# Performance work log

Hardware: AMD Instinct MI355X
Metric: run time of the kernel (lower is better)

Reference implementation:

```python
import jax, jax.numpy as jnp
import numpy as np

B, C, H, W = 4, 64, 64, 64

def setup_inputs() -> dict:
    key = jax.random.key(0)
    ks = jax.random.split(key, 9)
    return {
        "x": jax.random.normal(ks[0], (B, C, H, W), dtype=jnp.float32),
        "Wq": jax.random.normal(ks[1], (C, C), dtype=jnp.float32) * (1.0 / np.sqrt(C)),
        "bq": jax.random.normal(ks[2], (C,), dtype=jnp.float32) * 0.02,
        "Wk": jax.random.normal(ks[3], (C, C), dtype=jnp.float32) * (1.0 / np.sqrt(C)),
        "bk": jax.random.normal(ks[4], (C,), dtype=jnp.float32) * 0.02,
        "Wv": jax.random.normal(ks[5], (C, C), dtype=jnp.float32) * (1.0 / np.sqrt(C)),
        "bv": jax.random.normal(ks[6], (C,), dtype=jnp.float32) * 0.02,
        "rel_h": jax.random.normal(ks[7], (1, C, H, 1), dtype=jnp.float32),
        "rel_w": jax.random.normal(ks[8], (1, C, 1, W), dtype=jnp.float32),
    }

def reference(x, Wq, bq, Wk, bk, Wv, bv, rel_h, rel_w):
    b, c, h, w = x.shape
    n = h * w
    xf = x.reshape(b, c, n)                                  # [B,C,N]
    # 1x1 convs == channel-wise linear maps (weight [out,in])
    q = jnp.einsum('oc,bcn->bno', Wq, xf) + bq               # [B,N,C]
    k = jnp.einsum('oc,bcn->bon', Wk, xf) + bk[:, None]      # [B,C,N]
    v = jnp.einsum('oc,bcn->bon', Wv, xf) + bv[:, None]      # [B,C,N]
    energy = jnp.einsum('bnc,bcm->bnm', q, k)                # content term [B,N,N]
    pos = (rel_h + rel_w).reshape(c, n)                      # [C,N]
    energy = energy + jnp.einsum('bnc,cm->bnm', q, pos)      # add positional bias
    attn = jax.nn.softmax(energy, axis=-1)                   # [B,N,N]
    # out[b,c,n] = sum_m v[b,c,m] * attn[b,n,m]  (bmm with attention^T)
    out = jnp.einsum('bcm,bnm->bcn', v, attn)
    return out.reshape(b, c, h, w)
```

## Files before the change

### kernel.cpp

```cpp
#include <hip/hip_runtime.h>
#include <math.h>

#define NPOS 4096
#define NB   4
#define NROW (NB * NPOS)
#define LOG2E 1.44269504088896f

typedef _Float16 f16;
typedef f16 f16x4 __attribute__((ext_vector_type(4)));
typedef f16 f16x8 __attribute__((ext_vector_type(8)));
typedef float f32x4 __attribute__((ext_vector_type(4)));

#define LDW 72

__global__ __launch_bounds__(256) void qkv_proj(
    const float* __restrict__ x,
    const float* __restrict__ Wq, const float* __restrict__ bq,
    const float* __restrict__ Wk, const float* __restrict__ bk,
    const float* __restrict__ Wv, const float* __restrict__ bv,
    const float* __restrict__ rel_h, const float* __restrict__ rel_w,
    f16* __restrict__ qh, f16* __restrict__ kh, f16* __restrict__ vh)
{
    __shared__ __align__(16) f16 Ws[192 * LDW];
    __shared__ __align__(16) f16 Xs[32 * LDW];
    __shared__ __align__(16) f16 Vs[64 * 36];

    const int tid = threadIdx.x;
    const int b   = blockIdx.x >> 7;
    const int n0  = (blockIdx.x & 127) << 5;

    #pragma unroll
    for (int k = 0; k < 12; ++k) {
        int idx  = tid + k * 256;
        int orow = idx >> 4;
        int cseg = (idx & 15) << 2;
        int mat  = orow >> 6;
        int o    = orow & 63;
        const float* wsrc = (mat == 0) ? Wq : ((mat == 1) ? Wk : Wv);
        float4 v = *(const float4*)(wsrc + o * 64 + cseg);
        f16x4 h; h[0] = (f16)v.x; h[1] = (f16)v.y; h[2] = (f16)v.z; h[3] = (f16)v.w;
        *(f16x4*)(&Ws[orow * LDW + cseg]) = h;
    }
    {
        int c  = tid >> 2;
        int ns = (tid & 3) << 3;
        const float* xp = x + ((size_t)(b * 64 + c)) * NPOS + n0 + ns;
        float4 v0 = *(const float4*)(xp);
        float4 v1 = *(const float4*)(xp + 4);
        Xs[(ns + 0) * LDW + c] = (f16)v0.x;
        Xs[(ns + 1) * LDW + c] = (f16)v0.y;
        Xs[(ns + 2) * LDW + c] = (f16)v0.z;
        Xs[(ns + 3) * LDW + c] = (f16)v0.w;
        Xs[(ns + 4) * LDW + c] = (f16)v1.x;
        Xs[(ns + 5) * LDW + c] = (f16)v1.y;
        Xs[(ns + 6) * LDW + c] = (f16)v1.z;
        Xs[(ns + 7) * LDW + c] = (f16)v1.w;
    }
    __syncthreads();

    const int wave = tid >> 6;
    const int lane = tid & 63;
    const int quad = lane >> 4;
    const int l16  = lane & 15;
    const int rg   = wave >> 1;
    const int tb   = (wave & 1) * 6;

    const f16x8 a0 = *(const f16x8*)(&Xs[(rg * 16 + l16) * LDW + quad * 8]);
    const f16x8 a1 = *(const f16x8*)(&Xs[(rg * 16 + l16) * LDW + 32 + quad * 8]);

    f32x4 acc[6];
    #pragma unroll
    for (int i = 0; i < 6; ++i) {
        int t = tb + i;
        f32x4 c0 = {0, 0, 0, 0};
        f16x8 b0 = *(const f16x8*)(&Ws[(t * 16 + l16) * LDW + quad * 8]);
        f16x8 b1 = *(const f16x8*)(&Ws[(t * 16 + l16) * LDW + 32 + quad * 8]);
        c0 = __builtin_amdgcn_mfma_f32_16x16x32_f16(a0, b0, c0, 0, 0, 0);
        c0 = __builtin_amdgcn_mfma_f32_16x16x32_f16(a1, b1, c0, 0, 0, 0);
        acc[i] = c0;
    }

    #pragma unroll
    for (int i = 0; i < 6; ++i) {
        int t = tb + i;
        if (t < 4) {
            int o = t * 16 + l16;
            float bb = bq[o];
            #pragma unroll
            for (int r = 0; r < 4; ++r) {
                size_t n = (size_t)b * NPOS + n0 + rg * 16 + quad * 4 + r;
                qh[n * 64 + o] = (f16)((acc[i][r] + bb) * LOG2E);
            }
        } else if (t < 8) {
            int o = (t - 4) * 16 + l16;
            int h = n0 >> 6;
            int wbase = (n0 & 63) + rg * 16;
            float bb = bk[o] + rel_h[o * 64 + h];
            #pragma unroll
            for (int r = 0; r < 4; ++r) {
                size_t n = (size_t)b * NPOS + n0 + rg * 16 + quad * 4 + r;
                kh[n * 64 + o] = (f16)(acc[i][r] + bb + rel_w[o * 64 + wbase + quad * 4 + r]);
            }
        } else {
            int o = (t - 8) * 16 + l16;
            float bb = bv[o];
            #pragma unroll
            for (int r = 0; r < 4; ++r)
                Vs[o * 36 + rg * 16 + quad * 4 + r] = (f16)(acc[i][r] + bb);
        }
    }
    __syncthreads();
    {
        int c  = tid >> 2;
        int ns = (tid & 3) << 3;
        f16x8 vv = *(const f16x8*)(&Vs[c * 36 + ns]);
        *(f16x8*)(vh + ((size_t)(b * 64 + c)) * NPOS + n0 + ns) = vv;
    }
}

#define LDP 72

__global__ __launch_bounds__(256, 4) void attn(
    const f16* __restrict__ qh, const f16* __restrict__ kh,
    const f16* __restrict__ vh,
    f16* __restrict__ Op, float* __restrict__ Mp, float* __restrict__ Lp,
    int split, int mchunk)
{
    __shared__ __align__(16) f16 Ks[2][64 * LDP];
    __shared__ __align__(16) f16 Vt[2][64 * LDP];

    const int tid  = threadIdx.x;
    const int wave = tid >> 6;
    const int lane = tid & 63;
    const int quad = lane >> 4;
    const int l16  = lane & 15;
    const int s    = blockIdx.x % split;
    const int tile = blockIdx.x / split;
    const int b    = tile >> 5;
    const int n0   = (tile & 31) << 7;

    f16x8 bq0[2], bq1[2];
    #pragma unroll
    for (int g = 0; g < 2; ++g) {
        const f16* qbase = qh + ((size_t)b * NPOS + n0 + wave * 32 + g * 16 + l16) * 64;
        bq0[g] = *(const f16x8*)(qbase + quad * 8);
        bq1[g] = *(const f16x8*)(qbase + 32 + quad * 8);
    }

    f32x4 O[2][4] = {{{0,0,0,0},{0,0,0,0},{0,0,0,0},{0,0,0,0}},
                     {{0,0,0,0},{0,0,0,0},{0,0,0,0},{0,0,0,0}}};
    float m_i[2] = {-1e30f, -1e30f}, l_i[2] = {0.f, 0.f};

    const int srow = tid >> 2;
    const int sseg = (tid & 3) * 16;
    const f16* kb = kh + (size_t)b * NPOS * 64;
    const f16* vb = vh + (size_t)b * 64 * NPOS;

    const int m_begin = s * mchunk;
    for (int m0 = m_begin; m0 < m_begin + mchunk; m0 += 128) {
        #pragma unroll
        for (int h = 0; h < 2; ++h) {
            const f16* ksrc = kb + (size_t)(m0 + h * 64 + srow) * 64 + sseg;
            *(f16x8*)(&Ks[h][srow * LDP + sseg])     = *(const f16x8*)(ksrc);
            *(f16x8*)(&Ks[h][srow * LDP + sseg + 8]) = *(const f16x8*)(ksrc + 8);
            const f16* vsrc = vb + (size_t)srow * NPOS + m0 + h * 64 + sseg;
            *(f16x8*)(&Vt[h][srow * LDP + sseg])     = *(const f16x8*)(vsrc);
            *(f16x8*)(&Vt[h][srow * LDP + sseg + 8]) = *(const f16x8*)(vsrc + 8);
        }
        __syncthreads();

        #pragma unroll
        for (int h = 0; h < 2; ++h) {
            f32x4 S[2][4];
            #pragma unroll
            for (int t = 0; t < 4; ++t) {
                f16x8 ak0 = *(const f16x8*)(&Ks[h][(t * 16 + l16) * LDP + quad * 8]);
                f16x8 ak1 = *(const f16x8*)(&Ks[h][(t * 16 + l16) * LDP + 32 + quad * 8]);
                #pragma unroll
                for (int g = 0; g < 2; ++g) {
                    f32x4 acc = {0, 0, 0, 0};
                    acc = __builtin_amdgcn_mfma_f32_16x16x32_f16(ak0, bq0[g], acc, 0, 0, 0);
                    acc = __builtin_amdgcn_mfma_f32_16x16x32_f16(ak1, bq1[g], acc, 0, 0, 0);
                    S[g][t] = acc;
                }
            }

            f16x4 pa[2][4];
            #pragma unroll
            for (int g = 0; g < 2; ++g) {
                float mx = S[g][0][0];
                #pragma unroll
                for (int t = 0; t < 4; ++t)
                    #pragma unroll
                    for (int r = 0; r < 4; ++r) mx = fmaxf(mx, S[g][t][r]);
                mx = fmaxf(mx, __shfl_xor(mx, 16));
                mx = fmaxf(mx, __shfl_xor(mx, 32));

                if (__any(mx > m_i[g])) {
                    float mnew  = fmaxf(m_i[g], mx);
                    float alpha = __builtin_amdgcn_exp2f(m_i[g] - mnew);
                    m_i[g] = mnew;
                    l_i[g] *= alpha;
                    #pragma unroll
                    for (int r = 0; r < 4; ++r) {
                        float av = __shfl(alpha, quad * 20 + r);
                        O[g][0][r] *= av; O[g][1][r] *= av;
                        O[g][2][r] *= av; O[g][3][r] *= av;
                    }
                }

                float rs = 0.f;
                #pragma unroll
                for (int t = 0; t < 4; ++t) {
                    f16x4 a;
                    #pragma unroll
                    for (int r = 0; r < 4; ++r) {
                        float e = __builtin_amdgcn_exp2f(S[g][t][r] - m_i[g]);
                        rs += e;
                        a[r] = (f16)e;
                    }
                    pa[g][t] = a;
                }
                rs += __shfl_xor(rs, 16);
                rs += __shfl_xor(rs, 32);
                l_i[g] += rs;
            }

            #pragma unroll
            for (int u = 0; u < 4; ++u) {
                #pragma unroll
                for (int t = 0; t < 4; ++t) {
                    f16x4 bf = *(const f16x4*)(&Vt[h][(u * 16 + l16) * LDP + t * 16 + quad * 4]);
                    O[0][u] = __builtin_amdgcn_mfma_f32_16x16x16f16(pa[0][t], bf, O[0][u], 0, 0, 0);
                    O[1][u] = __builtin_amdgcn_mfma_f32_16x16x16f16(pa[1][t], bf, O[1][u], 0, 0, 0);
                }
            }
        }
        __syncthreads();
    }

    #pragma unroll
    for (int g = 0; g < 2; ++g) {
        #pragma unroll
        for (int r = 0; r < 4; ++r) {
            float lr  = __shfl(l_i[g], quad * 20 + r);
            float inv = 1.f / lr;
            size_t row = (size_t)b * NPOS + n0 + wave * 32 + g * 16 + quad * 4 + r;
            #pragma unroll
            for (int u = 0; u < 4; ++u)
                Op[((size_t)s * NROW + row) * 64 + u * 16 + l16] = (f16)(O[g][u][r] * inv);
        }
        if (lane < 16) {
            size_t row = (size_t)b * NPOS + n0 + wave * 32 + g * 16 + l16;
            Mp[(size_t)s * NROW + row] = m_i[g];
            Lp[(size_t)s * NROW + row] = l_i[g];
        }
    }
}

__global__ __launch_bounds__(256) void combine(
    const f16* __restrict__ Op, const float* __restrict__ Mp,
    const float* __restrict__ Lp, float* __restrict__ out, int split)
{
    __shared__ float Ot[16 * 68];

    const int tid = threadIdx.x;
    const int b   = blockIdx.x >> 8;
    const int n0  = (blockIdx.x & 255) << 4;

    {
        int nl = tid >> 4;
        int cs = (tid & 15) << 2;
        size_t row = (size_t)b * NPOS + n0 + nl;

        float M = -1e30f;
        for (int s2 = 0; s2 < split; ++s2)
            M = fmaxf(M, Mp[(size_t)s2 * NROW + row]);

        float L = 0.f;
        float val[4] = {0.f, 0.f, 0.f, 0.f};
        for (int s2 = 0; s2 < split; ++s2) {
            float w = Lp[(size_t)s2 * NROW + row] *
                      __builtin_amdgcn_exp2f(Mp[(size_t)s2 * NROW + row] - M);
            L += w;
            f16x4 o0 = *(const f16x4*)(Op + ((size_t)s2 * NROW + row) * 64 + cs);
            #pragma unroll
            for (int j = 0; j < 4; ++j) val[j] += w * (float)o0[j];
        }
        float invL = 1.f / L;
        float4 v4 = { val[0] * invL, val[1] * invL, val[2] * invL, val[3] * invL };
        *(float4*)(&Ot[nl * 68 + cs]) = v4;
    }
    __syncthreads();
    {
        int c  = tid >> 2;
        int ns = (tid & 3) << 2;
        float4 v4 = { Ot[(ns + 0) * 68 + c], Ot[(ns + 1) * 68 + c],
                      Ot[(ns + 2) * 68 + c], Ot[(ns + 3) * 68 + c] };
        *(float4*)(out + ((size_t)(b * 64 + c)) * NPOS + n0 + ns) = v4;
    }
}

extern "C" void kernel_launch(void* const* d_in, const int* in_sizes, int n_in,
                              void* d_out, int out_size, void* d_ws, size_t ws_size,
                              hipStream_t stream) {
    const float* x     = (const float*)d_in[0];
    const float* Wq    = (const float*)d_in[1];
    const float* bq    = (const float*)d_in[2];
    const float* Wk    = (const float*)d_in[3];
    const float* bk    = (const float*)d_in[4];
    const float* Wv    = (const float*)d_in[5];
    const float* bv    = (const float*)d_in[6];
    const float* rel_h = (const float*)d_in[7];
    const float* rel_w = (const float*)d_in[8];
    float* out = (float*)d_out;

    const size_t qkv_elems = (size_t)NROW * 64;
    int split = 8;
    {
        size_t need = 3 * qkv_elems * sizeof(f16)
                    + (size_t)split * NROW * 64 * sizeof(f16)
                    + 2 * (size_t)split * NROW * sizeof(float);
        if (ws_size < need) split = 4;
    }
    const int mchunk = NPOS / split;

    f16* qh = (f16*)d_ws;
    f16* kh = qh + qkv_elems;
    f16* vh = kh + qkv_elems;
    f16* Op = vh + qkv_elems;
    float* Mp = (float*)(Op + (size_t)split * NROW * 64);
    float* Lp = Mp + (size_t)split * NROW;

    qkv_proj<<<NB * (NPOS / 32), 256, 0, stream>>>(x, Wq, bq, Wk, bk, Wv, bv,
                                                   rel_h, rel_w, qh, kh, vh);
    attn<<<NB * (NPOS / 128) * split, 256, 0, stream>>>(qh, kh, vh, Op, Mp, Lp,
                                                        split, mchunk);
    combine<<<NB * (NPOS / 16), 256, 0, stream>>>(Op, Mp, Lp, out, split);
}
```

Before: 116.5 us.

## Double-buffer K/V tiles with register prefetch in attention loop

Measured after the change: 117.9 us. About the same (+1.1%).

```diff
diff --git a/kernel.cpp b/kernel.cpp
--- a/kernel.cpp
+++ b/kernel.cpp
@@ -157,86 +157,105 @@
     const f16* vb = vh + (size_t)b * 64 * NPOS;
 
     const int m_begin = s * mchunk;
-    for (int m0 = m_begin; m0 < m_begin + mchunk; m0 += 128) {
+    const int m_end   = m_begin + mchunk;
+
+    {
+        const f16* ksrc = kb + (size_t)(m_begin + srow) * 64 + sseg;
+        *(f16x8*)(&Ks[0][srow * LDP + sseg])     = *(const f16x8*)(ksrc);
+        *(f16x8*)(&Ks[0][srow * LDP + sseg + 8]) = *(const f16x8*)(ksrc + 8);
+        const f16* vsrc = vb + (size_t)srow * NPOS + m_begin + sseg;
+        *(f16x8*)(&Vt[0][srow * LDP + sseg])     = *(const f16x8*)(vsrc);
+        *(f16x8*)(&Vt[0][srow * LDP + sseg + 8]) = *(const f16x8*)(vsrc + 8);
+    }
+    __syncthreads();
+
+    int cur = 0;
+    for (int m0 = m_begin; m0 < m_end; m0 += 64) {
+        f16x8 kr0, kr1, vr0, vr1;
+        const bool have_next = (m0 + 64 < m_end);
+        if (have_next) {
+            const f16* ksrc = kb + (size_t)(m0 + 64 + srow) * 64 + sseg;
+            kr0 = *(const f16x8*)(ksrc);
+            kr1 = *(const f16x8*)(ksrc + 8);
+            const f16* vsrc = vb + (size_t)srow * NPOS + m0 + 64 + sseg;
+            vr0 = *(const f16x8*)(vsrc);
+            vr1 = *(const f16x8*)(vsrc + 8);
+        }
+
+        f32x4 S[2][4];
         #pragma unroll
-        for (int h = 0; h < 2; ++h) {
-            const f16* ksrc = kb + (size_t)(m0 + h * 64 + srow) * 64 + sseg;
-            *(f16x8*)(&Ks[h][srow * LDP + sseg])     = *(const f16x8*)(ksrc);
-            *(f16x8*)(&Ks[h][srow * LDP + sseg + 8]) = *(const f16x8*)(ksrc + 8);
-            const f16* vsrc = vb + (size_t)srow * NPOS + m0 + h * 64 + sseg;
-            *(f16x8*)(&Vt[h][srow * LDP + sseg])     = *(const f16x8*)(vsrc);
-            *(f16x8*)(&Vt[h][srow * LDP + sseg + 8]) = *(const f16x8*)(vsrc + 8);
-        }
-        __syncthreads();
-
+        for (int t = 0; t < 4; ++t) {
+            f16x8 ak0 = *(const f16x8*)(&Ks[cur][(t * 16 + l16) * LDP + quad * 8]);
+            f16x8 ak1 = *(const f16x8*)(&Ks[cur][(t * 16 + l16) * LDP + 32 + quad * 8]);
+            #pragma unroll
+            for (int g = 0; g < 2; ++g) {
+                f32x4 acc = {0, 0, 0, 0};
+                acc = __builtin_amdgcn_mfma_f32_16x16x32_f16(ak0, bq0[g], acc, 0, 0, 0);
+                acc = __builtin_amdgcn_mfma_f32_16x16x32_f16(ak1, bq1[g], acc, 0, 0, 0);
+                S[g][t] = acc;
+            }
+        }
+
+        f16x4 pa[2][4];
         #pragma unroll
-        for (int h = 0; h < 2; ++h) {
-            f32x4 S[2][4];
+        for (int g = 0; g < 2; ++g) {
+            float mx = S[g][0][0];
+            #pragma unroll
+            for (int t = 0; t < 4; ++t)
+                #pragma unroll
+                for (int r = 0; r < 4; ++r) mx = fmaxf(mx, S[g][t][r]);
+            mx = fmaxf(mx, __shfl_xor(mx, 16));
+            mx = fmaxf(mx, __shfl_xor(mx, 32));
+
+            if (__any(mx > m_i[g])) {
+                float mnew  = fmaxf(m_i[g], mx);
+                float alpha = __builtin_amdgcn_exp2f(m_i[g] - mnew);
+                m_i[g] = mnew;
+                l_i[g] *= alpha;
+                #pragma unroll
+                for (int r = 0; r < 4; ++r) {
+                    float av = __shfl(alpha, quad * 20 + r);
+                    O[g][0][r] *= av; O[g][1][r] *= av;
+                    O[g][2][r] *= av; O[g][3][r] *= av;
+                }
+            }
+
+            float rs = 0.f;
             #pragma unroll
             for (int t = 0; t < 4; ++t) {
-                f16x8 ak0 = *(const f16x8*)(&Ks[h][(t * 16 + l16) * LDP + quad * 8]);
-                f16x8 ak1 = *(const f16x8*)(&Ks[h][(t * 16 + l16) * LDP + 32 + quad * 8]);
+                f16x4 a;
                 #pragma unroll
-                for (int g = 0; g < 2; ++g) {
-                    f32x4 acc = {0, 0, 0, 0};
-                    acc = __builtin_amdgcn_mfma_f32_16x16x32_f16(ak0, bq0[g], acc, 0, 0, 0);
-                    acc = __builtin_amdgcn_mfma_f32_16x16x32_f16(ak1, bq1[g], acc, 0, 0, 0);
-                    S[g][t] = acc;
+                for (int r = 0; r < 4; ++r) {
+                    float e = __builtin_amdgcn_exp2f(S[g][t][r] - m_i[g]);
+                    rs += e;
+                    a[r] = (f16)e;
                 }
-            }
-
-            f16x4 pa[2][4];
-            #pragma unroll
-            for (int g = 0; g < 2; ++g) {
-                float mx = S[g][0][0];
-                #pragma unroll
-                for (int t = 0; t < 4; ++t)
-                    #pragma unroll
-                    for (int r = 0; r < 4; ++r) mx = fmaxf(mx, S[g][t][r]);
-                mx = fmaxf(mx, __shfl_xor(mx, 16));
-                mx = fmaxf(mx, __shfl_xor(mx, 32));
-
-                if (__any(mx > m_i[g])) {
-                    float mnew  = fmaxf(m_i[g], mx);
-                    float alpha = __builtin_amdgcn_exp2f(m_i[g] - mnew);
-                    m_i[g] = mnew;
-                    l_i[g] *= alpha;
-                    #pragma unroll
-                    for (int r = 0; r < 4; ++r) {
-                        float av = __shfl(alpha, quad * 20 + r);
-                        O[g][0][r] *= av; O[g][1][r] *= av;
-                        O[g][2][r] *= av; O[g][3][r] *= av;
-                    }
-                }
-
-                float rs = 0.f;
-                #pragma unroll
-                for (int t = 0; t < 4; ++t) {
-                    f16x4 a;
-                    #pragma unroll
-                    for (int r = 0; r < 4; ++r) {
-                        float e = __builtin_amdgcn_exp2f(S[g][t][r] - m_i[g]);
-                        rs += e;
-                        a[r] = (f16)e;
-                    }
-                    pa[g][t] = a;
-                }
-                rs += __shfl_xor(rs, 16);
-                rs += __shfl_xor(rs, 32);
-                l_i[g] += rs;
-            }
-
-            #pragma unroll
-            for (int u = 0; u < 4; ++u) {
-                #pragma unroll
-                for (int t = 0; t < 4; ++t) {
-                    f16x4 bf = *(const f16x4*)(&Vt[h][(u * 16 + l16) * LDP + t * 16 + quad * 4]);
-                    O[0][u] = __builtin_amdgcn_mfma_f32_16x16x16f16(pa[0][t], bf, O[0][u], 0, 0, 0);
-                    O[1][u] = __builtin_amdgcn_mfma_f32_16x16x16f16(pa[1][t], bf, O[1][u], 0, 0, 0);
-                }
-            }
-        }
-        __syncthreads();
+                pa[g][t] = a;
+            }
+            rs += __shfl_xor(rs, 16);
+            rs += __shfl_xor(rs, 32);
+            l_i[g] += rs;
+        }
+
+        #pragma unroll
+        for (int u = 0; u < 4; ++u) {
+            #pragma unroll
+            for (int t = 0; t < 4; ++t) {
+                f16x4 bf = *(const f16x4*)(&Vt[cur][(u * 16 + l16) * LDP + t * 16 + quad * 4]);
+                O[0][u] = __builtin_amdgcn_mfma_f32_16x16x16f16(pa[0][t], bf, O[0][u], 0, 0, 0);
+                O[1][u] = __builtin_amdgcn_mfma_f32_16x16x16f16(pa[1][t], bf, O[1][u], 0, 0, 0);
+            }
+        }
+
+        if (have_next) {
+            int nxt = cur ^ 1;
+            *(f16x8*)(&Ks[nxt][srow * LDP + sseg])     = kr0;
+            *(f16x8*)(&Ks[nxt][srow * LDP + sseg + 8]) = kr1;
+            *(f16x8*)(&Vt[nxt][srow * LDP + sseg])     = vr0;
+            *(f16x8*)(&Vt[nxt][srow * LDP + sseg + 8]) = vr1;
+            __syncthreads();
+        }
+        cur ^= 1;
     }
 
     #pragma unroll
```

## Stage K/V via direct global-to-LDS loads with XOR swizzle and 64-key tiles

Applied to the files above, without the earlier changes.

New measurement: 118.0 us. About the same (+1.3%).

```diff
diff --git a/kernel.cpp b/kernel.cpp
--- a/kernel.cpp
+++ b/kernel.cpp
@@ -10,6 +10,11 @@
 typedef f16 f16x4 __attribute__((ext_vector_type(4)));
 typedef f16 f16x8 __attribute__((ext_vector_type(8)));
 typedef float f32x4 __attribute__((ext_vector_type(4)));
+
+#define GLOAD_LDS16(g, l)                                                \
+    __builtin_amdgcn_global_load_lds(                                    \
+        (__attribute__((address_space(1))) void*)(g),                    \
+        (__attribute__((address_space(3))) void*)(l), 16, 0, 0)
 
 #define LDW 72
 
@@ -118,16 +123,14 @@
     }
 }
 
-#define LDP 72
-
 __global__ __launch_bounds__(256, 4) void attn(
     const f16* __restrict__ qh, const f16* __restrict__ kh,
     const f16* __restrict__ vh,
     f16* __restrict__ Op, float* __restrict__ Mp, float* __restrict__ Lp,
     int split, int mchunk)
 {
-    __shared__ __align__(16) f16 Ks[2][64 * LDP];
-    __shared__ __align__(16) f16 Vt[2][64 * LDP];
+    __shared__ __align__(16) f16 Ks[64 * 64];
+    __shared__ __align__(16) f16 Vt[64 * 64];
 
     const int tid  = threadIdx.x;
     const int wave = tid >> 6;
@@ -151,89 +154,90 @@
                      {{0,0,0,0},{0,0,0,0},{0,0,0,0},{0,0,0,0}}};
     float m_i[2] = {-1e30f, -1e30f}, l_i[2] = {0.f, 0.f};
 
-    const int srow = tid >> 2;
-    const int sseg = (tid & 3) * 16;
+    const int srow0 = wave * 16 + (lane >> 3);
+    const int srow1 = srow0 + 8;
+    const int jc    = lane & 7;
+    const int koff0 = ((jc ^ (srow0 & 7)) << 3);
+    const int koff1 = ((jc ^ (srow1 & 7)) << 3);
+    f16* ldsK0 = &Ks[(wave * 16 + 0) * 64];
+    f16* ldsK1 = &Ks[(wave * 16 + 8) * 64];
+    f16* ldsV0 = &Vt[(wave * 16 + 0) * 64];
+    f16* ldsV1 = &Vt[(wave * 16 + 8) * 64];
+
     const f16* kb = kh + (size_t)b * NPOS * 64;
     const f16* vb = vh + (size_t)b * 64 * NPOS;
 
     const int m_begin = s * mchunk;
-    for (int m0 = m_begin; m0 < m_begin + mchunk; m0 += 128) {
+    for (int m0 = m_begin; m0 < m_begin + mchunk; m0 += 64) {
+        GLOAD_LDS16(kb + (size_t)(m0 + srow0) * 64 + koff0, ldsK0);
+        GLOAD_LDS16(kb + (size_t)(m0 + srow1) * 64 + koff1, ldsK1);
+        GLOAD_LDS16(vb + (size_t)srow0 * NPOS + m0 + koff0, ldsV0);
+        GLOAD_LDS16(vb + (size_t)srow1 * NPOS + m0 + koff1, ldsV1);
+        __syncthreads();
+
+        f32x4 S[2][4];
         #pragma unroll
-        for (int h = 0; h < 2; ++h) {
-            const f16* ksrc = kb + (size_t)(m0 + h * 64 + srow) * 64 + sseg;
-            *(f16x8*)(&Ks[h][srow * LDP + sseg])     = *(const f16x8*)(ksrc);
-            *(f16x8*)(&Ks[h][srow * LDP + sseg + 8]) = *(const f16x8*)(ksrc + 8);
-            const f16* vsrc = vb + (size_t)srow * NPOS + m0 + h * 64 + sseg;
-            *(f16x8*)(&Vt[h][srow * LDP + sseg])     = *(const f16x8*)(vsrc);
-            *(f16x8*)(&Vt[h][srow * LDP + sseg + 8]) = *(const f16x8*)(vsrc + 8);
-        }
-        __syncthreads();
-
+        for (int t = 0; t < 4; ++t) {
+            f16x8 ak0 = *(const f16x8*)(&Ks[(t * 16 + l16) * 64 + ((quad ^ (l16 & 7)) << 3)]);
+            f16x8 ak1 = *(const f16x8*)(&Ks[(t * 16 + l16) * 64 + (((4 + quad) ^ (l16 & 7)) << 3)]);
+            #pragma unroll
+            for (int g = 0; g < 2; ++g) {
+                f32x4 acc = {0, 0, 0, 0};
+                acc = __builtin_amdgcn_mfma_f32_16x16x32_f16(ak0, bq0[g], acc, 0, 0, 0);
+                acc = __builtin_amdgcn_mfma_f32_16x16x32_f16(ak1, bq1[g], acc, 0, 0, 0);
+                S[g][t] = acc;
+            }
+        }
+
+        f16x4 pa[2][4];
         #pragma unroll
-        for (int h = 0; h < 2; ++h) {
-            f32x4 S[2][4];
+        for (int g = 0; g < 2; ++g) {
+            float mx = S[g][0][0];
+            #pragma unroll
+            for (int t = 0; t < 4; ++t)
+                #pragma unroll
+                for (int r = 0; r < 4; ++r) mx = fmaxf(mx, S[g][t][r]);
+            mx = fmaxf(mx, __shfl_xor(mx, 16));
+            mx = fmaxf(mx, __shfl_xor(mx, 32));
+
+            if (__any(mx > m_i[g])) {
+                float mnew  = fmaxf(m_i[g], mx);
+                float alpha = __builtin_amdgcn_exp2f(m_i[g] - mnew);
+                m_i[g] = mnew;
+                l_i[g] *= alpha;
+                #pragma unroll
+                for (int r = 0; r < 4; ++r) {
+                    float av = __shfl(alpha, quad * 20 + r);
+                    O[g][0][r] *= av; O[g][1][r] *= av;
+                    O[g][2][r] *= av; O[g][3][r] *= av;
+                }
+            }
+
+            float rs = 0.f;
             #pragma unroll
             for (int t = 0; t < 4; ++t) {
-                f16x8 ak0 = *(const f16x8*)(&Ks[h][(t * 16 + l16) * LDP + quad * 8]);
-                f16x8 ak1 = *(const f16x8*)(&Ks[h][(t * 16 + l16) * LDP + 32 + quad * 8]);
+                f16x4 a;
                 #pragma unroll
-                for (int g = 0; g < 2; ++g) {
-                    f32x4 acc = {0, 0, 0, 0};
-                    acc = __builtin_amdgcn_mfma_f32_16x16x32_f16(ak0, bq0[g], acc, 0, 0, 0);
-                    acc = __builtin_amdgcn_mfma_f32_16x16x32_f16(ak1, bq1[g], acc, 0, 0, 0);
-                    S[g][t] = acc;
+                for (int r = 0; r < 4; ++r) {
+                    float e = __builtin_amdgcn_exp2f(S[g][t][r] - m_i[g]);
+                    rs += e;
+                    a[r] = (f16)e;
                 }
-            }
-
-            f16x4 pa[2][4];
-            #pragma unroll
-            for (int g = 0; g < 2; ++g) {
-                float mx = S[g][0][0];
-                #pragma unroll
-                for (int t = 0; t < 4; ++t)
-                    #pragma unroll
-                    for (int r = 0; r < 4; ++r) mx = fmaxf(mx, S[g][t][r]);
-                mx = fmaxf(mx, __shfl_xor(mx, 16));
-                mx = fmaxf(mx, __shfl_xor(mx, 32));
-
-                if (__any(mx > m_i[g])) {
-                    float mnew  = fmaxf(m_i[g], mx);
-                    float alpha = __builtin_amdgcn_exp2f(m_i[g] - mnew);
-                    m_i[g] = mnew;
-                    l_i[g] *= alpha;
-                    #pragma unroll
-                    for (int r = 0; r < 4; ++r) {
-                        float av = __shfl(alpha, quad * 20 + r);
-                        O[g][0][r] *= av; O[g][1][r] *= av;
-                        O[g][2][r] *= av; O[g][3][r] *= av;
-                    }
-                }
-
-                float rs = 0.f;
-                #pragma unroll
-                for (int t = 0; t < 4; ++t) {
-                    f16x4 a;
-                    #pragma unroll
-                    for (int r = 0; r < 4; ++r) {
-                        float e = __builtin_amdgcn_exp2f(S[g][t][r] - m_i[g]);
-                        rs += e;
-                        a[r] = (f16)e;
-                    }
-                    pa[g][t] = a;
-                }
-                rs += __shfl_xor(rs, 16);
-                rs += __shfl_xor(rs, 32);
-                l_i[g] += rs;
-            }
-
-            #pragma unroll
-            for (int u = 0; u < 4; ++u) {
-                #pragma unroll
-                for (int t = 0; t < 4; ++t) {
-                    f16x4 bf = *(const f16x4*)(&Vt[h][(u * 16 + l16) * LDP + t * 16 + quad * 4]);
-                    O[0][u] = __builtin_amdgcn_mfma_f32_16x16x16f16(pa[0][t], bf, O[0][u], 0, 0, 0);
-                    O[1][u] = __builtin_amdgcn_mfma_f32_16x16x16f16(pa[1][t], bf, O[1][u], 0, 0, 0);
-                }
+                pa[g][t] = a;
+            }
+            rs += __shfl_xor(rs, 16);
+            rs += __shfl_xor(rs, 32);
+            l_i[g] += rs;
+        }
+
+        #pragma unroll
+        for (int u = 0; u < 4; ++u) {
+            #pragma unroll
+            for (int t = 0; t < 4; ++t) {
+                int slot = (((2 * t + (quad >> 1)) ^ (l16 & 7)) << 3) + (quad & 1) * 4;
+                f16x4 bf = *(const f16x4*)(&Vt[(u * 16 + l16) * 64 + slot]);
+                O[0][u] = __builtin_amdgcn_mfma_f32_16x16x16f16(pa[0][t], bf, O[0][u], 0, 0, 0);
+                O[1][u] = __builtin_amdgcn_mfma_f32_16x16x16f16(pa[1][t], bf, O[1][u], 0, 0, 0);
             }
         }
         __syncthreads();
@@ -243,12 +247,10 @@
     for (int g = 0; g < 2; ++g) {
         #pragma unroll
         for (int r = 0; r < 4; ++r) {
-            float lr  = __shfl(l_i[g], quad * 20 + r);
-            float inv = 1.f / lr;
             size_t row = (size_t)b * NPOS + n0 + wave * 32 + g * 16 + quad * 4 + r;
             #pragma unroll
             for (int u = 0; u < 4; ++u)
-                Op[((size_t)s * NROW + row) * 64 + u * 16 + l16] = (f16)(O[g][u][r] * inv);
+                Op[((size_t)s * NROW + row) * 64 + u * 16 + l16] = (f16)O[g][u][r];
         }
         if (lane < 16) {
             size_t row = (size_t)b * NPOS + n0 + wave * 32 + g * 16 + l16;
@@ -280,12 +282,11 @@
         float L = 0.f;
         float val[4] = {0.f, 0.f, 0.f, 0.f};
         for (int s2 = 0; s2 < split; ++s2) {
-            float w = Lp[(size_t)s2 * NROW + row] *
-                      __builtin_amdgcn_exp2f(Mp[(size_t)s2 * NROW + row] - M);
-            L += w;
+            float e = __builtin_amdgcn_exp2f(Mp[(size_t)s2 * NROW + row] - M);
+            L += Lp[(size_t)s2 * NROW + row] * e;
             f16x4 o0 = *(const f16x4*)(Op + ((size_t)s2 * NROW + row) * 64 + cs);
             #pragma unroll
-            for (int j = 0; j < 4; ++j) val[j] += w * (float)o0[j];
+            for (int j = 0; j < 4; ++j) val[j] += e * (float)o0[j];
         }
         float invL = 1.f / L;
         float4 v4 = { val[0] * invL, val[1] * invL, val[2] * invL, val[3] * invL };
```
